# Performance work log

Measured on AMD Instinct MI355X. Metric: run time of the kernel, lower is better.

Reference implementation:

```python
import jax, jax.numpy as jnp
import numpy as np

VP = 0.4
EP = 0.21

def _c_matrix():
    # Faithfully replicate the original Ci (including its asymmetric rows 2) and invert.
    Ci = np.zeros((6, 6), dtype=np.float64)
    Ci[0, 0] = 1 / EP; Ci[0, 1] = -VP / EP; Ci[0, 2] = -VP / EP
    Ci[1, 0] = -VP / EP; Ci[1, 1] = 1 / EP; Ci[1, 2] = -VP / EP
    Ci[2, 0] = -VP;      Ci[2, 1] = -VP;      Ci[2, 2] = 1 / EP
    Ci[3, 3] = 2 * (1 + VP) / EP
    Ci[4, 4] = 2 * (1 + VP) / EP
    Ci[5, 5] = 2 * (1 + VP) / EP
    return np.linalg.inv(Ci).astype(np.float32)

C_MAT = jnp.asarray(_c_matrix())
N = 12288

def setup_inputs() -> dict:
    key = jax.random.key(0)
    k1, k2, k3 = jax.random.split(key, 3)
    xyz = jax.random.normal(k1, (N, 3), dtype=jnp.float32)
    new_xyz = jax.random.normal(k2, (N, 3), dtype=jnp.float32)
    # ~half the points are 'inside' (gt_sdf < 1e-8)
    gt_sdf = jax.random.uniform(k3, (N,), dtype=jnp.float32) - 0.5
    return {"new_xyz": new_xyz, "xyz": xyz, "gt_sdf": gt_sdf}

def reference(new_xyz, xyz, gt_sdf):
    motion = new_xyz - xyz                      # [N,3]
    inside = gt_sdf < 1e-8                      # [N] bool, selects inside points
    w = new_xyz                                 # warped coordinates (KNN space)
    n = w.shape[0]
    # Brute-force NN among inside points (KDTree k=2, second neighbor == nearest non-self).
    sq = jnp.sum(w * w, axis=1)                 # [N]
    d2 = sq[:, None] + sq[None, :] - 2.0 * (w @ w.T)   # [N,N] squared distances
    BIG = jnp.float32(1e30)
    bad_col = (~inside)[None, :] | jnp.eye(n, dtype=bool)
    d2 = jnp.where(bad_col, BIG, d2)
    nn_idx = jnp.argmin(d2, axis=1)             # nearest inside neighbor (excluding self)
    nn_d = jnp.sqrt(jnp.maximum(jnp.min(d2, axis=1), 0.0))
    # tree_list1 filter: drop rows whose nearest neighbor is a duplicate point
    valid = inside & (nn_d > 1e-8)              # [N]
    dm = motion[nn_idx] - motion                # motion_delta
    dc = w[nn_idx] - w + 1e-8                   # cords_delta (+1e-8 as in original)
    v = valid[:, None]
    dm = jnp.where(v, dm, 0.0)                  # neutralize masked rows (keep shapes static)
    dc = jnp.where(v, dc, 1.0)
    du, dv, dw = dm[:, 0], dm[:, 1], dm[:, 2]
    dx, dy, dz = dc[:, 0], dc[:, 1], dc[:, 2]
    et = jnp.stack([du / dx, dv / dy, dw / dz,
                    (du / dy + dv / dx) / 2,
                    (du / dz + dw / dx) / 2,
                    (dw / dy + dv / dz) / 2], axis=1)   # [N,6] strain tensor
    # diag(et @ C @ et.T) as an O(N) batched quadratic form
    q = jnp.einsum('ni,ij,nj->n', et, C_MAT, et)
    q = jnp.where(valid, q, 0.0)
    n_valid = jnp.sum(valid).astype(jnp.float32)
    return jnp.linalg.norm(q) / n_valid
```

## Files before the change

kernel.cpp:

```cpp
#include <hip/hip_runtime.h>
#include <math.h>
#include <string.h>

#define N 12288
#define QP 7168
#define TILE 128
#define NSPLIT 56
#define ACCS 2
#define QBLK 512
#define NQB 14
#define NBLK (NQB * NSPLIT)
#define BT 1024
#define BB 12
#define NPART (QP / 256)

typedef unsigned long long ull;

struct CMat { float c[6][6]; };

__global__ __launch_bounds__(1024) void build_kernel(
    const float* __restrict__ new_xyz,
    const float* __restrict__ gt_sdf,
    float4* __restrict__ pts,
    int* __restrict__ cj,
    int* __restrict__ Mout,
    ull* __restrict__ best,
    unsigned int* __restrict__ ticket2,
    unsigned int* __restrict__ ticket3)
{
    const int tid = threadIdx.x;
    const int b = blockIdx.x;
    const int lane = tid & 63;
    const int wave = tid >> 6;

    int cpre = 0;
    #pragma unroll
    for (int r = 0; r < BB - 1; ++r) {
        const float sv = (r < b) ? gt_sdf[r * BT + tid] : 1.0f;
        cpre += (sv < 1e-8f) ? 1 : 0;
    }
    #pragma unroll
    for (int off = 32; off > 0; off >>= 1)
        cpre += __shfl_down(cpre, off, 64);

    const int idx = b * BT + tid;
    const float px = new_xyz[3 * idx + 0];
    const float py = new_xyz[3 * idx + 1];
    const float pz = new_xyz[3 * idx + 2];
    const bool ins = gt_sdf[idx] < 1e-8f;
    const ull m = __ballot(ins);
    const int rank = __popcll(m & ((1ull << lane) - 1ull));

    __shared__ int wpre[16];
    __shared__ int wcnt[16];
    __shared__ int woff[16];
    __shared__ int tot_s;
    if (lane == 0) { wpre[wave] = cpre; wcnt[wave] = __popcll(m); }
    __syncthreads();
    if (tid == 0) {
        int cb = 0;
        for (int w = 0; w < 16; ++w) cb += wpre[w];
        int run = cb;
        for (int w = 0; w < 16; ++w) { woff[w] = run; run += wcnt[w]; }
        tot_s = run;
    }
    __syncthreads();

    const int slot = woff[wave] + rank;
    if (ins && slot < QP) {
        pts[slot] = make_float4(-2.0f * px, -2.0f * py, -2.0f * pz,
                                px * px + py * py + pz * pz);
        cj[slot] = idx;
    }

    const int gid = b * BT + tid;
    if (gid < QP) best[gid] = ~0ull;
    if (gid == 0) { *ticket2 = 0u; *ticket3 = 0u; }

    if (b == BB - 1) {
        const int M = tot_s;
        if (tid == 0) *Mout = M;
        for (int s = M + tid; s < QP; s += BT)
            pts[s] = make_float4(0.0f, 0.0f, 0.0f, 3e30f);
    }
}

template<bool CAREFUL>
__device__ __forceinline__ void nn_inner(
    const float4* __restrict__ tile,
    const float* wx, const float* wy, const float* wz,
    const int* kx,
    float* bd, int* bk)
{
    #pragma unroll 8
    for (int k = 0; k < TILE; ++k) {
        const float4 b = tile[k];
        #pragma unroll
        for (int a = 0; a < ACCS; ++a) {
            float t = fmaf(wz[a], b.z, b.w);
            t = fmaf(wy[a], b.y, t);
            t = fmaf(wx[a], b.x, t);
            bool ok = t < bd[a];
            if (CAREFUL) ok = ok && (k != kx[a]);
            if (ok) { bd[a] = t; bk[a] = k; }
        }
    }
}

__global__ __launch_bounds__(256, 4) void nn_loss_kernel(
    const float* __restrict__ new_xyz,
    const float* __restrict__ xyz,
    const float4* __restrict__ pts,
    const int* __restrict__ cj,
    const int* __restrict__ Mptr,
    ull* __restrict__ best,
    unsigned int* __restrict__ ticket2,
    unsigned int* __restrict__ ticket3,
    double* __restrict__ partial_sum,
    unsigned int* __restrict__ partial_cnt,
    float* __restrict__ out,
    CMat C)
{
    const int tid = threadIdx.x;
    const int f = blockIdx.x;
    const int qb = f % NQB;
    const int s = f / NQB;
    const int qbase = qb * QBLK;
    const int jb = s * TILE;
    const int M = *Mptr;

    if (jb < M && qbase < M) {
        float wx[ACCS], wy[ACCS], wz[ACCS];
        int kx[ACCS];
        #pragma unroll
        for (int a = 0; a < ACCS; ++a) {
            const int ci = qbase + tid + a * 256;
            const float4 q = pts[ci];
            wx[a] = -0.5f * q.x;
            wy[a] = -0.5f * q.y;
            wz[a] = -0.5f * q.z;
            kx[a] = ci - jb;
        }

        __shared__ float4 tile[TILE];
        if (tid < TILE) tile[tid] = pts[jb + tid];
        __syncthreads();

        float bd[ACCS];
        int bk[ACCS];
        #pragma unroll
        for (int a = 0; a < ACCS; ++a) { bd[a] = 3.0e38f; bk[a] = 0; }

        const bool dirty = (jb < qbase + QBLK) && (jb + TILE > qbase);
        if (dirty)
            nn_inner<true>(tile, wx, wy, wz, kx, bd, bk);
        else
            nn_inner<false>(tile, wx, wy, wz, kx, bd, bk);

        #pragma unroll
        for (int a = 0; a < ACCS; ++a) {
            const int ci = qbase + tid + a * 256;
            unsigned u = __float_as_uint(bd[a]);
            u = ((int)u < 0) ? ~u : (u | 0x80000000u);
            const ull v = ((ull)u << 32) | (ull)(unsigned)(jb + bk[a]);
            atomicMin(&best[ci], v);
        }
    }

    __syncthreads();
    if (tid == 0) {
        __threadfence();
        __hip_atomic_fetch_add(ticket2, 1u, __ATOMIC_RELEASE,
                               __HIP_MEMORY_SCOPE_AGENT);
    }
    if (f >= NPART) return;

    if (tid == 0) {
        long long guard = 0;
        while (__hip_atomic_load(ticket2, __ATOMIC_ACQUIRE,
                                 __HIP_MEMORY_SCOPE_AGENT) < (unsigned)NBLK) {
            __builtin_amdgcn_s_sleep(8);
            if (++guard > (1ll << 28)) break;
        }
    }
    __syncthreads();

    const int ci = f * 256 + tid;
    const ull b64 = best[ci];
    const bool real = (ci < M);

    const unsigned u = (unsigned)(b64 >> 32);
    const unsigned bits = (u & 0x80000000u) ? (u ^ 0x80000000u) : ~u;
    const float key = __uint_as_float(bits);
    const int cc = real ? (int)(unsigned)(b64 & 0xffffffffu) : 0;

    const int i  = real ? cj[ci] : 0;
    const int nn = cj[cc];

    const float wix = new_xyz[3 * i + 0];
    const float wiy = new_xyz[3 * i + 1];
    const float wiz = new_xyz[3 * i + 2];
    const float sqi = wix * wix + wiy * wiy + wiz * wiz;

    const float d2 = sqi + key;
    const float nnd = sqrtf(fmaxf(d2, 0.0f));
    const bool valid = real && (nnd > 1e-8f);

    float q = 0.0f;
    if (valid) {
        const float xix = xyz[3 * i + 0], xiy = xyz[3 * i + 1], xiz = xyz[3 * i + 2];
        const float wnx = new_xyz[3 * nn + 0], wny = new_xyz[3 * nn + 1], wnz = new_xyz[3 * nn + 2];
        const float xnx = xyz[3 * nn + 0],     xny = xyz[3 * nn + 1],     xnz = xyz[3 * nn + 2];

        const float du = (wnx - xnx) - (wix - xix);
        const float dv = (wny - xny) - (wiy - xiy);
        const float dw = (wnz - xnz) - (wiz - xiz);
        const float dx = wnx - wix + 1e-8f;
        const float dy = wny - wiy + 1e-8f;
        const float dz = wnz - wiz + 1e-8f;

        float et[6];
        et[0] = du / dx;
        et[1] = dv / dy;
        et[2] = dw / dz;
        et[3] = (du / dy + dv / dx) * 0.5f;
        et[4] = (du / dz + dw / dx) * 0.5f;
        et[5] = (dw / dy + dv / dz) * 0.5f;

        #pragma unroll
        for (int a = 0; a < 6; ++a) {
            float s2 = 0.0f;
            #pragma unroll
            for (int b2 = 0; b2 < 6; ++b2) s2 += C.c[a][b2] * et[b2];
            q += et[a] * s2;
        }
    }

    double q2 = (double)q * (double)q;
    #pragma unroll
    for (int off = 32; off > 0; off >>= 1)
        q2 += __shfl_down(q2, off, 64);
    const ull vm = __ballot(valid);
    const int lane = tid & 63;
    const int wid = tid >> 6;

    __shared__ double wsum[4];
    __shared__ unsigned wcnt2[4];
    __shared__ bool sdone;
    if (lane == 0) { wsum[wid] = q2; wcnt2[wid] = (unsigned)__popcll(vm); }
    __syncthreads();
    if (tid == 0) {
        partial_sum[f] = wsum[0] + wsum[1] + wsum[2] + wsum[3];
        partial_cnt[f] = wcnt2[0] + wcnt2[1] + wcnt2[2] + wcnt2[3];
        __threadfence();
        const unsigned t = atomicAdd(ticket3, 1u);
        sdone = (t == NPART - 1);
    }
    __syncthreads();

    if (sdone && tid < 64) {
        __threadfence();
        double ss = (tid < NPART) ? partial_sum[tid] : 0.0;
        double cc2 = (tid < NPART) ? (double)partial_cnt[tid] : 0.0;
        #pragma unroll
        for (int off = 32; off > 0; off >>= 1) {
            ss += __shfl_down(ss, off, 64);
            cc2 += __shfl_down(cc2, off, 64);
        }
        if (tid == 0) out[0] = (float)(sqrt(ss) / cc2);
    }
}

static void build_cmat(CMat* M)
{
    const double VP = 0.4, EP = 0.21;
    double A[6][12];
    memset(A, 0, sizeof(A));
    double Ci[6][6];
    memset(Ci, 0, sizeof(Ci));
    Ci[0][0] = 1.0 / EP; Ci[0][1] = -VP / EP; Ci[0][2] = -VP / EP;
    Ci[1][0] = -VP / EP; Ci[1][1] = 1.0 / EP; Ci[1][2] = -VP / EP;
    Ci[2][0] = -VP;      Ci[2][1] = -VP;      Ci[2][2] = 1.0 / EP;
    Ci[3][3] = 2.0 * (1.0 + VP) / EP;
    Ci[4][4] = Ci[3][3];
    Ci[5][5] = Ci[3][3];

    for (int i = 0; i < 6; ++i) {
        for (int j = 0; j < 6; ++j) A[i][j] = Ci[i][j];
        A[i][6 + i] = 1.0;
    }
    for (int col = 0; col < 6; ++col) {
        int piv = col;
        for (int r = col + 1; r < 6; ++r)
            if (fabs(A[r][col]) > fabs(A[piv][col])) piv = r;
        if (piv != col)
            for (int c = 0; c < 12; ++c) { double t = A[col][c]; A[col][c] = A[piv][c]; A[piv][c] = t; }
        const double d = A[col][col];
        for (int c = 0; c < 12; ++c) A[col][c] /= d;
        for (int r = 0; r < 6; ++r) {
            if (r == col) continue;
            const double f = A[r][col];
            if (f == 0.0) continue;
            for (int c = 0; c < 12; ++c) A[r][c] -= f * A[col][c];
        }
    }
    for (int i = 0; i < 6; ++i)
        for (int j = 0; j < 6; ++j)
            M->c[i][j] = (float)A[i][6 + j];
}

extern "C" void kernel_launch(void* const* d_in, const int* in_sizes, int n_in,
                              void* d_out, int out_size, void* d_ws, size_t ws_size,
                              hipStream_t stream)
{
    const float* new_xyz = (const float*)d_in[0];
    const float* xyz     = (const float*)d_in[1];
    const float* gt_sdf  = (const float*)d_in[2];
    float* out = (float*)d_out;

    char* p = (char*)d_ws;
    float4* pts = (float4*)p;                    p += (size_t)QP * 16;
    int* cj = (int*)p;                           p += (size_t)QP * 4;
    int* Mptr = (int*)p;                         p += 16;
    ull* best = (ull*)p;                         p += (size_t)QP * 8;
    double* partial_sum = (double*)p;            p += NPART * sizeof(double);
    unsigned int* partial_cnt = (unsigned int*)p; p += NPART * sizeof(unsigned int);
    unsigned int* ticket2 = (unsigned int*)p;    p += sizeof(unsigned int);
    unsigned int* ticket3 = (unsigned int*)p;

    CMat C;
    build_cmat(&C);

    build_kernel<<<BB, BT, 0, stream>>>(new_xyz, gt_sdf, pts, cj, Mptr, best,
                                        ticket2, ticket3);
    nn_loss_kernel<<<NBLK, 256, 0, stream>>>(new_xyz, xyz, pts, cj, Mptr, best,
                                             ticket2, ticket3,
                                             partial_sum, partial_cnt, out, C);
}
```

Measured before the change: 93.86 us.

## Fuse compaction scan into NN kernel and replace atomics/spin-wait with partial-result reduction

Drops the separate build kernel. Every NN block now scans gt_sdf itself and packs only the query and tile points it needs into shared memory. Instead of a 64-bit atomicMin plus a grid-wide spin barrier, each split writes its per-query best to a [NSPLIT, QP] buffer, and a second kernel reduces over splits and computes the loss. This removes one launch, the atomics and the spin-wait. In exchange, every one of the 784 blocks redoes a 12288-element scan, and extra global traffic goes to the packed buffer.

```diff
diff --git a/kernel.cpp b/kernel.cpp
--- a/kernel.cpp
+++ b/kernel.cpp
@@ -10,79 +10,49 @@
 #define QBLK 512
 #define NQB 14
 #define NBLK (NQB * NSPLIT)
-#define BT 1024
-#define BB 12
+#define SCAN_R (N / 256)
 #define NPART (QP / 256)
 
 typedef unsigned long long ull;
 
 struct CMat { float c[6][6]; };
 
-__global__ __launch_bounds__(1024) void build_kernel(
-    const float* __restrict__ new_xyz,
-    const float* __restrict__ gt_sdf,
-    float4* __restrict__ pts,
-    int* __restrict__ cj,
-    int* __restrict__ Mout,
-    ull* __restrict__ best,
-    unsigned int* __restrict__ ticket2,
-    unsigned int* __restrict__ ticket3)
-{
-    const int tid = threadIdx.x;
-    const int b = blockIdx.x;
-    const int lane = tid & 63;
-    const int wave = tid >> 6;
-
-    int cpre = 0;
-    #pragma unroll
-    for (int r = 0; r < BB - 1; ++r) {
-        const float sv = (r < b) ? gt_sdf[r * BT + tid] : 1.0f;
-        cpre += (sv < 1e-8f) ? 1 : 0;
-    }
-    #pragma unroll
-    for (int off = 32; off > 0; off >>= 1)
-        cpre += __shfl_down(cpre, off, 64);
-
-    const int idx = b * BT + tid;
-    const float px = new_xyz[3 * idx + 0];
-    const float py = new_xyz[3 * idx + 1];
-    const float pz = new_xyz[3 * idx + 2];
-    const bool ins = gt_sdf[idx] < 1e-8f;
-    const ull m = __ballot(ins);
-    const int rank = __popcll(m & ((1ull << lane) - 1ull));
-
-    __shared__ int wpre[16];
-    __shared__ int wcnt[16];
-    __shared__ int woff[16];
-    __shared__ int tot_s;
-    if (lane == 0) { wpre[wave] = cpre; wcnt[wave] = __popcll(m); }
-    __syncthreads();
-    if (tid == 0) {
-        int cb = 0;
-        for (int w = 0; w < 16; ++w) cb += wpre[w];
-        int run = cb;
-        for (int w = 0; w < 16; ++w) { woff[w] = run; run += wcnt[w]; }
-        tot_s = run;
-    }
-    __syncthreads();
-
-    const int slot = woff[wave] + rank;
-    if (ins && slot < QP) {
-        pts[slot] = make_float4(-2.0f * px, -2.0f * py, -2.0f * pz,
-                                px * px + py * py + pz * pz);
-        cj[slot] = idx;
-    }
-
-    const int gid = b * BT + tid;
-    if (gid < QP) best[gid] = ~0ull;
-    if (gid == 0) { *ticket2 = 0u; *ticket3 = 0u; }
-
-    if (b == BB - 1) {
-        const int M = tot_s;
-        if (tid == 0) *Mout = M;
-        for (int s = M + tid; s < QP; s += BT)
-            pts[s] = make_float4(0.0f, 0.0f, 0.0f, 3e30f);
-    }
+__device__ __forceinline__ void scan_flags(
+    const float* __restrict__ gt_sdf, int tid, int lane, int w4,
+    ull* flags_out, int* spref , int* scratch4 ,
+    int* M_out)
+{
+    ull flags = 0;
+    #pragma unroll 8
+    for (int r = 0; r < SCAN_R; ++r)
+        if (gt_sdf[r * 256 + tid] < 1e-8f) flags |= (1ull << r);
+
+    #pragma unroll 8
+    for (int r = 0; r < SCAN_R; ++r) {
+        const ull m = __ballot((unsigned)((flags >> r) & 1ull));
+        if (lane == 0) spref[r * 4 + w4] = __popcll(m);
+    }
+    __syncthreads();
+
+    const int c = (tid < SCAN_R * 4) ? spref[tid] : 0;
+    int inc = c;
+    #pragma unroll
+    for (int off = 1; off < 64; off <<= 1) {
+        const int v = __shfl_up(inc, off, 64);
+        if (lane >= off) inc += v;
+    }
+    if (lane == 63) scratch4[w4] = inc;
+    __syncthreads();
+    int wofs = 0;
+    for (int w = 0; w < w4; ++w) wofs += scratch4[w];
+    const int excl = wofs + inc - c;
+    const int Mtot = scratch4[0] + scratch4[1] + scratch4[2] + scratch4[3];
+    __syncthreads();
+    if (tid < SCAN_R * 4) spref[tid] = excl;
+    __syncthreads();
+
+    *flags_out = flags;
+    *M_out = Mtot;
 }
 
 template<bool CAREFUL>
@@ -107,95 +77,141 @@
     }
 }
 
-__global__ __launch_bounds__(256, 4) void nn_loss_kernel(
+__global__ __launch_bounds__(256, 4) void nn_pack_kernel(
     const float* __restrict__ new_xyz,
-    const float* __restrict__ xyz,
-    const float4* __restrict__ pts,
-    const int* __restrict__ cj,
-    const int* __restrict__ Mptr,
-    ull* __restrict__ best,
-    unsigned int* __restrict__ ticket2,
-    unsigned int* __restrict__ ticket3,
-    double* __restrict__ partial_sum,
-    unsigned int* __restrict__ partial_cnt,
-    float* __restrict__ out,
-    CMat C)
+    const float* __restrict__ gt_sdf,
+    ull* __restrict__ packed,
+    unsigned int* __restrict__ ticket3)
 {
     const int tid = threadIdx.x;
     const int f = blockIdx.x;
+    const int lane = tid & 63;
+    const int w4 = tid >> 6;
     const int qb = f % NQB;
     const int s = f / NQB;
     const int qbase = qb * QBLK;
     const int jb = s * TILE;
-    const int M = *Mptr;
-
-    if (jb < M && qbase < M) {
-        float wx[ACCS], wy[ACCS], wz[ACCS];
-        int kx[ACCS];
-        #pragma unroll
-        for (int a = 0; a < ACCS; ++a) {
-            const int ci = qbase + tid + a * 256;
-            const float4 q = pts[ci];
-            wx[a] = -0.5f * q.x;
-            wy[a] = -0.5f * q.y;
-            wz[a] = -0.5f * q.z;
-            kx[a] = ci - jb;
-        }
-
-        __shared__ float4 tile[TILE];
-        if (tid < TILE) tile[tid] = pts[jb + tid];
-        __syncthreads();
-
-        float bd[ACCS];
-        int bk[ACCS];
-        #pragma unroll
-        for (int a = 0; a < ACCS; ++a) { bd[a] = 3.0e38f; bk[a] = 0; }
-
-        const bool dirty = (jb < qbase + QBLK) && (jb + TILE > qbase);
-        if (dirty)
-            nn_inner<true>(tile, wx, wy, wz, kx, bd, bk);
-        else
-            nn_inner<false>(tile, wx, wy, wz, kx, bd, bk);
-
-        #pragma unroll
-        for (int a = 0; a < ACCS; ++a) {
-            const int ci = qbase + tid + a * 256;
-            unsigned u = __float_as_uint(bd[a]);
-            u = ((int)u < 0) ? ~u : (u | 0x80000000u);
-            const ull v = ((ull)u << 32) | (ull)(unsigned)(jb + bk[a]);
-            atomicMin(&best[ci], v);
-        }
-    }
-
-    __syncthreads();
-    if (tid == 0) {
-        __threadfence();
-        __hip_atomic_fetch_add(ticket2, 1u, __ATOMIC_RELEASE,
-                               __HIP_MEMORY_SCOPE_AGENT);
-    }
-    if (f >= NPART) return;
-
-    if (tid == 0) {
-        long long guard = 0;
-        while (__hip_atomic_load(ticket2, __ATOMIC_ACQUIRE,
-                                 __HIP_MEMORY_SCOPE_AGENT) < (unsigned)NBLK) {
-            __builtin_amdgcn_s_sleep(8);
-            if (++guard > (1ll << 28)) break;
-        }
-    }
-    __syncthreads();
-
+
+    __shared__ int spref[SCAN_R * 4];
+    __shared__ int scratch4[4];
+    __shared__ float qx[QBLK], qy[QBLK], qz[QBLK];
+    __shared__ float4 tile[TILE];
+
+    ull flags;
+    int M;
+    scan_flags(gt_sdf, tid, lane, w4, &flags, spref, scratch4, &M);
+
+    if (f == 0 && tid == 0) *ticket3 = 0u;
+
+    if (jb >= M || qbase >= M) return;
+
+    for (int t = tid; t < QBLK; t += 256) { qx[t] = 0.0f; qy[t] = 0.0f; qz[t] = 0.0f; }
+    if (tid < TILE) tile[tid] = make_float4(0.0f, 0.0f, 0.0f, 3e30f);
+    __syncthreads();
+
+    for (int r = 0; r < SCAN_R; ++r) {
+        const ull m = __ballot((unsigned)((flags >> r) & 1ull));
+        if ((flags >> r) & 1ull) {
+            const int rank = __popcll(m & ((1ull << lane) - 1ull));
+            const int slot = spref[r * 4 + w4] + rank;
+            const bool inq = (slot >= qbase) && (slot < qbase + QBLK);
+            const bool intl = (slot >= jb) && (slot < jb + TILE);
+            if (inq || intl) {
+                const int idx = r * 256 + tid;
+                const float x = new_xyz[3 * idx + 0];
+                const float y = new_xyz[3 * idx + 1];
+                const float z = new_xyz[3 * idx + 2];
+                if (inq) { qx[slot - qbase] = x; qy[slot - qbase] = y; qz[slot - qbase] = z; }
+                if (intl) tile[slot - jb] = make_float4(-2.0f * x, -2.0f * y, -2.0f * z,
+                                                        x * x + y * y + z * z);
+            }
+        }
+    }
+    __syncthreads();
+
+    float wx[ACCS], wy[ACCS], wz[ACCS];
+    int kx[ACCS];
+    #pragma unroll
+    for (int a = 0; a < ACCS; ++a) {
+        const int t = tid + a * 256;
+        wx[a] = qx[t];
+        wy[a] = qy[t];
+        wz[a] = qz[t];
+        kx[a] = qbase + t - jb;
+    }
+
+    float bd[ACCS];
+    int bk[ACCS];
+    #pragma unroll
+    for (int a = 0; a < ACCS; ++a) { bd[a] = 3.0e38f; bk[a] = 0; }
+
+    const bool dirty = (jb < qbase + QBLK) && (jb + TILE > qbase);
+    if (dirty)
+        nn_inner<true>(tile, wx, wy, wz, kx, bd, bk);
+    else
+        nn_inner<false>(tile, wx, wy, wz, kx, bd, bk);
+
+    #pragma unroll
+    for (int a = 0; a < ACCS; ++a) {
+        const int ci = qbase + tid + a * 256;
+        unsigned u = __float_as_uint(bd[a]);
+        u = ((int)u < 0) ? ~u : (u | 0x80000000u);
+        packed[(size_t)s * QP + ci] = ((ull)u << 32) | (ull)(unsigned)(jb + bk[a]);
+    }
+}
+
+__global__ __launch_bounds__(256) void loss_kernel(
+    const float* __restrict__ new_xyz,
+    const float* __restrict__ xyz,
+    const float* __restrict__ gt_sdf,
+    const ull* __restrict__ packed,
+    double* __restrict__ partial_sum,
+    unsigned int* __restrict__ partial_cnt,
+    unsigned int* __restrict__ ticket3,
+    float* __restrict__ out,
+    CMat C)
+{
+    const int tid = threadIdx.x;
+    const int f = blockIdx.x;
+    const int lane = tid & 63;
+    const int w4 = tid >> 6;
+
+    __shared__ int spref[SCAN_R * 4];
+    __shared__ int scratch4[4];
+    __shared__ int cj_lds[QP];
+
+    ull flags;
+    int M;
+    scan_flags(gt_sdf, tid, lane, w4, &flags, spref, scratch4, &M);
+
+    for (int r = 0; r < SCAN_R; ++r) {
+        const ull m = __ballot((unsigned)((flags >> r) & 1ull));
+        if ((flags >> r) & 1ull) {
+            const int rank = __popcll(m & ((1ull << lane) - 1ull));
+            const int slot = spref[r * 4 + w4] + rank;
+            if (slot < QP) cj_lds[slot] = r * 256 + tid;
+        }
+    }
+    __syncthreads();
+
+    const int ns_eff = (M + TILE - 1) / TILE > NSPLIT ? NSPLIT : (M + TILE - 1) / TILE;
     const int ci = f * 256 + tid;
-    const ull b64 = best[ci];
+
+    ull best = ~0ull;
+    #pragma unroll 8
+    for (int s2 = 0; s2 < ns_eff; ++s2) {
+        const ull p = packed[(size_t)s2 * QP + ci];
+        best = (p < best) ? p : best;
+    }
+
     const bool real = (ci < M);
-
-    const unsigned u = (unsigned)(b64 >> 32);
+    const unsigned u = (unsigned)(best >> 32);
     const unsigned bits = (u & 0x80000000u) ? (u ^ 0x80000000u) : ~u;
     const float key = __uint_as_float(bits);
-    const int cc = real ? (int)(unsigned)(b64 & 0xffffffffu) : 0;
-
-    const int i  = real ? cj[ci] : 0;
-    const int nn = cj[cc];
+    const int cc = real ? (int)(unsigned)(best & 0xffffffffu) : 0;
+
+    const int i  = real ? cj_lds[ci] : 0;
+    const int nn = cj_lds[cc];
 
     const float wix = new_xyz[3 * i + 0];
     const float wiy = new_xyz[3 * i + 1];
@@ -241,13 +257,11 @@
     for (int off = 32; off > 0; off >>= 1)
         q2 += __shfl_down(q2, off, 64);
     const ull vm = __ballot(valid);
-    const int lane = tid & 63;
-    const int wid = tid >> 6;
 
     __shared__ double wsum[4];
     __shared__ unsigned wcnt2[4];
     __shared__ bool sdone;
-    if (lane == 0) { wsum[wid] = q2; wcnt2[wid] = (unsigned)__popcll(vm); }
+    if (lane == 0) { wsum[w4] = q2; wcnt2[w4] = (unsigned)__popcll(vm); }
     __syncthreads();
     if (tid == 0) {
         partial_sum[f] = wsum[0] + wsum[1] + wsum[2] + wsum[3];
@@ -299,9 +313,9 @@
         for (int c = 0; c < 12; ++c) A[col][c] /= d;
         for (int r = 0; r < 6; ++r) {
             if (r == col) continue;
-            const double f = A[r][col];
-            if (f == 0.0) continue;
-            for (int c = 0; c < 12; ++c) A[r][c] -= f * A[col][c];
+            const double fc = A[r][col];
+            if (fc == 0.0) continue;
+            for (int c = 0; c < 12; ++c) A[r][c] -= fc * A[col][c];
         }
     }
     for (int i = 0; i < 6; ++i)
@@ -319,21 +333,16 @@
     float* out = (float*)d_out;
 
     char* p = (char*)d_ws;
-    float4* pts = (float4*)p;                    p += (size_t)QP * 16;
-    int* cj = (int*)p;                           p += (size_t)QP * 4;
-    int* Mptr = (int*)p;                         p += 16;
-    ull* best = (ull*)p;                         p += (size_t)QP * 8;
-    double* partial_sum = (double*)p;            p += NPART * sizeof(double);
+    ull* packed = (ull*)p;                        p += (size_t)NSPLIT * QP * 8;
+    double* partial_sum = (double*)p;             p += NPART * sizeof(double);
     unsigned int* partial_cnt = (unsigned int*)p; p += NPART * sizeof(unsigned int);
-    unsigned int* ticket2 = (unsigned int*)p;    p += sizeof(unsigned int);
     unsigned int* ticket3 = (unsigned int*)p;
 
     CMat C;
     build_cmat(&C);
 
-    build_kernel<<<BB, BT, 0, stream>>>(new_xyz, gt_sdf, pts, cj, Mptr, best,
-                                        ticket2, ticket3);
-    nn_loss_kernel<<<NBLK, 256, 0, stream>>>(new_xyz, xyz, pts, cj, Mptr, best,
-                                             ticket2, ticket3,
-                                             partial_sum, partial_cnt, out, C);
-}
+    nn_pack_kernel<<<NBLK, 256, 0, stream>>>(new_xyz, gt_sdf, packed, ticket3);
+    loss_kernel<<<NPART, 256, 0, stream>>>(new_xyz, xyz, gt_sdf, packed,
+                                           partial_sum, partial_cnt, ticket3,
+                                           out, C);
+}
```

New measurement: 91.99 us. 1.02x faster.

## Replace global spin-barrier with per-query-block last-arriver finalization

Applied to the files above, without the earlier changes.

Drops the grid-wide spin wait, in which the first blocks polled a global ticket until all blocks finished. Each query block now has its own arrival counter, and the last of the NSPLIT column blocks to finish a query block computes the strain loss for its 512 queries. The final reduction then runs over NQB arrivals. This removes the spin-wait and its reliance on blocks being co-resident, and lets the epilogue overlap with NN work still running on other query blocks. In exchange, the epilogue runs on fewer blocks, each handling two 256-row chunks.

```diff
diff --git a/kernel.cpp b/kernel.cpp
--- a/kernel.cpp
+++ b/kernel.cpp
@@ -9,7 +9,6 @@
 #define ACCS 2
 #define QBLK 512
 #define NQB 14
-#define NBLK (NQB * NSPLIT)
 #define BT 1024
 #define BB 12
 #define NPART (QP / 256)
@@ -25,8 +24,8 @@
     int* __restrict__ cj,
     int* __restrict__ Mout,
     ull* __restrict__ best,
-    unsigned int* __restrict__ ticket2,
-    unsigned int* __restrict__ ticket3)
+    unsigned int* __restrict__ done,
+    unsigned int* __restrict__ ticket)
 {
     const int tid = threadIdx.x;
     const int b = blockIdx.x;
@@ -75,7 +74,8 @@
 
     const int gid = b * BT + tid;
     if (gid < QP) best[gid] = ~0ull;
-    if (gid == 0) { *ticket2 = 0u; *ticket3 = 0u; }
+    if (gid < NQB) done[gid] = 0u;
+    if (gid == NQB) *ticket = 0u;
 
     if (b == BB - 1) {
         const int M = tot_s;
@@ -114,20 +114,26 @@
     const int* __restrict__ cj,
     const int* __restrict__ Mptr,
     ull* __restrict__ best,
-    unsigned int* __restrict__ ticket2,
-    unsigned int* __restrict__ ticket3,
+    unsigned int* __restrict__ done,
+    unsigned int* __restrict__ ticket,
     double* __restrict__ partial_sum,
     unsigned int* __restrict__ partial_cnt,
     float* __restrict__ out,
     CMat C)
 {
     const int tid = threadIdx.x;
-    const int f = blockIdx.x;
-    const int qb = f % NQB;
-    const int s = f / NQB;
+    const int qb = blockIdx.x;
+    const int s = blockIdx.y;
     const int qbase = qb * QBLK;
     const int jb = s * TILE;
+    const int lane = tid & 63;
+    const int wid = tid >> 6;
     const int M = *Mptr;
+
+    __shared__ float4 tile[TILE];
+    __shared__ bool swin, sdone;
+    __shared__ double wsum[4];
+    __shared__ unsigned wcnt2[4];
 
     if (jb < M && qbase < M) {
         float wx[ACCS], wy[ACCS], wz[ACCS];
@@ -142,7 +148,6 @@
             kx[a] = ci - jb;
         }
 
-        __shared__ float4 tile[TILE];
         if (tid < TILE) tile[tid] = pts[jb + tid];
         __syncthreads();
 
@@ -170,91 +175,85 @@
     __syncthreads();
     if (tid == 0) {
         __threadfence();
-        __hip_atomic_fetch_add(ticket2, 1u, __ATOMIC_RELEASE,
-                               __HIP_MEMORY_SCOPE_AGENT);
-    }
-    if (f >= NPART) return;
+        const unsigned t = atomicAdd(&done[qb], 1u);
+        swin = (t == NSPLIT - 1);
+    }
+    __syncthreads();
+    if (!swin) return;
+
+    __threadfence();
+
+    #pragma unroll
+    for (int a = 0; a < 2; ++a) {
+        const int ci = qbase + a * 256 + tid;
+        const ull b64 = best[ci];
+        const bool real = (ci < M);
+
+        const unsigned u = (unsigned)(b64 >> 32);
+        const unsigned bits = (u & 0x80000000u) ? (u ^ 0x80000000u) : ~u;
+        const float key = __uint_as_float(bits);
+        const int cc = real ? (int)(unsigned)(b64 & 0xffffffffu) : 0;
+
+        const int i  = real ? cj[ci] : 0;
+        const int nn = cj[cc];
+
+        const float wix = new_xyz[3 * i + 0];
+        const float wiy = new_xyz[3 * i + 1];
+        const float wiz = new_xyz[3 * i + 2];
+        const float sqi = wix * wix + wiy * wiy + wiz * wiz;
+
+        const float d2 = sqi + key;
+        const float nnd = sqrtf(fmaxf(d2, 0.0f));
+        const bool valid = real && (nnd > 1e-8f);
+
+        float q = 0.0f;
+        if (valid) {
+            const float xix = xyz[3 * i + 0], xiy = xyz[3 * i + 1], xiz = xyz[3 * i + 2];
+            const float wnx = new_xyz[3 * nn + 0], wny = new_xyz[3 * nn + 1], wnz = new_xyz[3 * nn + 2];
+            const float xnx = xyz[3 * nn + 0],     xny = xyz[3 * nn + 1],     xnz = xyz[3 * nn + 2];
+
+            const float du = (wnx - xnx) - (wix - xix);
+            const float dv = (wny - xny) - (wiy - xiy);
+            const float dw = (wnz - xnz) - (wiz - xiz);
+            const float dx = wnx - wix + 1e-8f;
+            const float dy = wny - wiy + 1e-8f;
+            const float dz = wnz - wiz + 1e-8f;
+
+            float et[6];
+            et[0] = du / dx;
+            et[1] = dv / dy;
+            et[2] = dw / dz;
+            et[3] = (du / dy + dv / dx) * 0.5f;
+            et[4] = (du / dz + dw / dx) * 0.5f;
+            et[5] = (dw / dy + dv / dz) * 0.5f;
+
+            #pragma unroll
+            for (int aa = 0; aa < 6; ++aa) {
+                float s2 = 0.0f;
+                #pragma unroll
+                for (int b2 = 0; b2 < 6; ++b2) s2 += C.c[aa][b2] * et[b2];
+                q += et[aa] * s2;
+            }
+        }
+
+        double q2 = (double)q * (double)q;
+        #pragma unroll
+        for (int off = 32; off > 0; off >>= 1)
+            q2 += __shfl_down(q2, off, 64);
+        const ull vm = __ballot(valid);
+        if (lane == 0) { wsum[wid] = q2; wcnt2[wid] = (unsigned)__popcll(vm); }
+        __syncthreads();
+        if (tid == 0) {
+            partial_sum[2 * qb + a] = wsum[0] + wsum[1] + wsum[2] + wsum[3];
+            partial_cnt[2 * qb + a] = wcnt2[0] + wcnt2[1] + wcnt2[2] + wcnt2[3];
+        }
+        __syncthreads();
+    }
 
     if (tid == 0) {
-        long long guard = 0;
-        while (__hip_atomic_load(ticket2, __ATOMIC_ACQUIRE,
-                                 __HIP_MEMORY_SCOPE_AGENT) < (unsigned)NBLK) {
-            __builtin_amdgcn_s_sleep(8);
-            if (++guard > (1ll << 28)) break;
-        }
-    }
-    __syncthreads();
-
-    const int ci = f * 256 + tid;
-    const ull b64 = best[ci];
-    const bool real = (ci < M);
-
-    const unsigned u = (unsigned)(b64 >> 32);
-    const unsigned bits = (u & 0x80000000u) ? (u ^ 0x80000000u) : ~u;
-    const float key = __uint_as_float(bits);
-    const int cc = real ? (int)(unsigned)(b64 & 0xffffffffu) : 0;
-
-    const int i  = real ? cj[ci] : 0;
-    const int nn = cj[cc];
-
-    const float wix = new_xyz[3 * i + 0];
-    const float wiy = new_xyz[3 * i + 1];
-    const float wiz = new_xyz[3 * i + 2];
-    const float sqi = wix * wix + wiy * wiy + wiz * wiz;
-
-    const float d2 = sqi + key;
-    const float nnd = sqrtf(fmaxf(d2, 0.0f));
-    const bool valid = real && (nnd > 1e-8f);
-
-    float q = 0.0f;
-    if (valid) {
-        const float xix = xyz[3 * i + 0], xiy = xyz[3 * i + 1], xiz = xyz[3 * i + 2];
-        const float wnx = new_xyz[3 * nn + 0], wny = new_xyz[3 * nn + 1], wnz = new_xyz[3 * nn + 2];
-        const float xnx = xyz[3 * nn + 0],     xny = xyz[3 * nn + 1],     xnz = xyz[3 * nn + 2];
-
-        const float du = (wnx - xnx) - (wix - xix);
-        const float dv = (wny - xny) - (wiy - xiy);
-        const float dw = (wnz - xnz) - (wiz - xiz);
-        const float dx = wnx - wix + 1e-8f;
-        const float dy = wny - wiy + 1e-8f;
-        const float dz = wnz - wiz + 1e-8f;
-
-        float et[6];
-        et[0] = du / dx;
-        et[1] = dv / dy;
-        et[2] = dw / dz;
-        et[3] = (du / dy + dv / dx) * 0.5f;
-        et[4] = (du / dz + dw / dx) * 0.5f;
-        et[5] = (dw / dy + dv / dz) * 0.5f;
-
-        #pragma unroll
-        for (int a = 0; a < 6; ++a) {
-            float s2 = 0.0f;
-            #pragma unroll
-            for (int b2 = 0; b2 < 6; ++b2) s2 += C.c[a][b2] * et[b2];
-            q += et[a] * s2;
-        }
-    }
-
-    double q2 = (double)q * (double)q;
-    #pragma unroll
-    for (int off = 32; off > 0; off >>= 1)
-        q2 += __shfl_down(q2, off, 64);
-    const ull vm = __ballot(valid);
-    const int lane = tid & 63;
-    const int wid = tid >> 6;
-
-    __shared__ double wsum[4];
-    __shared__ unsigned wcnt2[4];
-    __shared__ bool sdone;
-    if (lane == 0) { wsum[wid] = q2; wcnt2[wid] = (unsigned)__popcll(vm); }
-    __syncthreads();
-    if (tid == 0) {
-        partial_sum[f] = wsum[0] + wsum[1] + wsum[2] + wsum[3];
-        partial_cnt[f] = wcnt2[0] + wcnt2[1] + wcnt2[2] + wcnt2[3];
         __threadfence();
-        const unsigned t = atomicAdd(ticket3, 1u);
-        sdone = (t == NPART - 1);
+        const unsigned t = atomicAdd(ticket, 1u);
+        sdone = (t == NQB - 1);
     }
     __syncthreads();
 
@@ -325,15 +324,15 @@
     ull* best = (ull*)p;                         p += (size_t)QP * 8;
     double* partial_sum = (double*)p;            p += NPART * sizeof(double);
     unsigned int* partial_cnt = (unsigned int*)p; p += NPART * sizeof(unsigned int);
-    unsigned int* ticket2 = (unsigned int*)p;    p += sizeof(unsigned int);
-    unsigned int* ticket3 = (unsigned int*)p;
+    unsigned int* done = (unsigned int*)p;       p += NQB * sizeof(unsigned int);
+    unsigned int* ticket = (unsigned int*)p;
 
     CMat C;
     build_cmat(&C);
 
     build_kernel<<<BB, BT, 0, stream>>>(new_xyz, gt_sdf, pts, cj, Mptr, best,
-                                        ticket2, ticket3);
-    nn_loss_kernel<<<NBLK, 256, 0, stream>>>(new_xyz, xyz, pts, cj, Mptr, best,
-                                             ticket2, ticket3,
-                                             partial_sum, partial_cnt, out, C);
-}
+                                        done, ticket);
+    nn_loss_kernel<<<dim3(NQB, NSPLIT), 256, 0, stream>>>(
+        new_xyz, xyz, pts, cj, Mptr, best, done, ticket,
+        partial_sum, partial_cnt, out, C);
+}
```

After: 89.30 us. 1.05x faster.
